# Kernel optimization log

Measured on AMD Instinct MI355X. Metric: run time of the kernel, lower is better.

The kernel has to match this reference:

```python
import jax, jax.numpy as jnp
import numpy as np

B, S, E, H = 2, 512, 1024, 16
D = E // H  # 64


def setup_inputs() -> dict:
    key = jax.random.key(0)
    ks = jax.random.split(key, 8)
    q = jax.random.normal(ks[0], (B, S, E), dtype=jnp.float32)
    k = jax.random.normal(ks[1], (B, S, E), dtype=jnp.float32)
    v = jax.random.normal(ks[2], (B, S, E), dtype=jnp.float32)
    # per-position bilinear term, scaled down so scores stay in a sane range
    p = jax.random.normal(ks[3], (B, S, H, D, D), dtype=jnp.float32) * 0.05
    # causal additive mask [S, S]
    neg = jnp.float32(-1e9)
    mask = jnp.where(jnp.triu(jnp.ones((S, S), dtype=bool), k=1), neg, jnp.float32(0.0))
    scale = 1.0 / np.sqrt(E)
    Wq = jax.random.normal(ks[4], (E, E), dtype=jnp.float32) * scale
    Wk = jax.random.normal(ks[5], (E, E), dtype=jnp.float32) * scale
    Wv = jax.random.normal(ks[6], (E, E), dtype=jnp.float32) * scale
    Wo = jax.random.normal(ks[7], (E, E), dtype=jnp.float32) * scale
    return {"q": q, "k": k, "v": v, "p": p, "mask": mask,
            "Wq": Wq, "Wk": Wk, "Wv": Wv, "Wo": Wo}


def reference(q, k, v, p, mask, Wq, Wk, Wv, Wo):
    b, s, e = q.shape
    h, d = p.shape[2], p.shape[3]
    # projections (torch Linear: y = x @ W.T), split into heads -> [b,h,s,d]
    qh = (q @ Wq.T).reshape(b, s, h, d).transpose(0, 2, 1, 3)
    kh = (k @ Wk.T).reshape(b, -1, h, d).transpose(0, 2, 1, 3)
    vh = (v @ Wv.T).reshape(b, -1, h, d).transpose(0, 2, 1, 3)
    # scores = einsum('bhse,bshef,bhtf->bhst') done in two steps
    qp = jnp.einsum('bhse,bshef->bhsf', qh, p)          # [b,h,s,d]
    scores = jnp.einsum('bhsf,bhtf->bhst', qp, kh)      # [b,h,s,t]
    scores = scores / jnp.sqrt(jnp.float32(d))
    scores = scores + mask[None, None, :, :]
    w = jax.nn.softmax(scores, axis=-1)
    att = jnp.einsum('bhst,bhtd->bshd', w, vh).reshape(b, s, e)
    return att @ Wo.T
```

## Files before the change

kernel.cpp:

```cpp
#include <hip/hip_runtime.h>
#include <hip/hip_bf16.h>

namespace {

constexpr int kB = 2, kS = 512, kE = 1024, kH = 16, kD = 64;
constexpr int kM = kB * kS;
constexpr int kBH = kB * kH;
constexpr int kSP = 524;

typedef short bf16x8 __attribute__((ext_vector_type(8)));
typedef float f32x4 __attribute__((ext_vector_type(4)));

__device__ __forceinline__ unsigned short f2bf(float f) {
  __hip_bfloat16 h = __float2bfloat16(f);
  unsigned short u;
  __builtin_memcpy(&u, &h, 2);
  return u;
}
__device__ __forceinline__ float bf2f(unsigned short u) {
  unsigned int x = (unsigned int)u << 16;
  float f;
  __builtin_memcpy(&f, &x, 4);
  return f;
}

__global__ void cvt7_kernel(const float* __restrict__ s0, const float* __restrict__ s1,
                            const float* __restrict__ s2, const float* __restrict__ s3,
                            const float* __restrict__ s4, const float* __restrict__ s5,
                            const float* __restrict__ s6,
                            unsigned short* __restrict__ dstBase) {
  const float* srcs[7] = {s0, s1, s2, s3, s4, s5, s6};
  const float* src = srcs[blockIdx.y];
  unsigned short* dst = dstBase + (size_t)blockIdx.y * (kM * kE);
  int i = (blockIdx.x * blockDim.x + threadIdx.x) * 4;
  float4 v = *reinterpret_cast<const float4*>(src + i);
  ushort4 o;
  o.x = f2bf(v.x); o.y = f2bf(v.y); o.z = f2bf(v.z); o.w = f2bf(v.w);
  *reinterpret_cast<ushort4*>(dst + i) = o;
}

__device__ __forceinline__ void mfma_tile_32x32(
    const unsigned short* __restrict__ A, int lda,
    const unsigned short* __restrict__ Bm, int ldb,
    int row0, int col0, int K, f32x4 acc[2][2]) {
  const int lane = threadIdx.x & 63;
  const int r = lane & 15;
  const int ko = (lane >> 4) * 8;
  const unsigned short* a0 = A + (size_t)(row0 + r) * lda + ko;
  const unsigned short* a1 = a0 + 16 * (size_t)lda;
  const unsigned short* b0 = Bm + (size_t)(col0 + r) * ldb + ko;
  const unsigned short* b1 = b0 + 16 * (size_t)ldb;
  for (int kk = 0; kk < K; kk += 32) {
    bf16x8 af0 = *reinterpret_cast<const bf16x8*>(a0 + kk);
    bf16x8 af1 = *reinterpret_cast<const bf16x8*>(a1 + kk);
    bf16x8 bg0 = *reinterpret_cast<const bf16x8*>(b0 + kk);
    bf16x8 bg1 = *reinterpret_cast<const bf16x8*>(b1 + kk);
    acc[0][0] = __builtin_amdgcn_mfma_f32_16x16x32_bf16(af0, bg0, acc[0][0], 0, 0, 0);
    acc[0][1] = __builtin_amdgcn_mfma_f32_16x16x32_bf16(af0, bg1, acc[0][1], 0, 0, 0);
    acc[1][0] = __builtin_amdgcn_mfma_f32_16x16x32_bf16(af1, bg0, acc[1][0], 0, 0, 0);
    acc[1][1] = __builtin_amdgcn_mfma_f32_16x16x32_bf16(af1, bg1, acc[1][1], 0, 0, 0);
  }
}

__global__ void proj_kernel(const unsigned short* __restrict__ qb,
                            const unsigned short* __restrict__ kb,
                            const unsigned short* __restrict__ vb,
                            const unsigned short* __restrict__ Wq,
                            const unsigned short* __restrict__ Wk,
                            const unsigned short* __restrict__ Wv,
                            unsigned short* __restrict__ qh,
                            unsigned short* __restrict__ kh,
                            unsigned short* __restrict__ vhT) {
  const int which = blockIdx.z;
  const unsigned short* A = which == 0 ? qb : (which == 1 ? kb : vb);
  const unsigned short* W = which == 0 ? Wq : (which == 1 ? Wk : Wv);
  const int row0 = blockIdx.y * 32, col0 = blockIdx.x * 32;
  f32x4 acc[2][2] = {};
  mfma_tile_32x32(A, kE, W, kE, row0, col0, kE, acc);
  const int lane = threadIdx.x & 63;
#pragma unroll
  for (int ri = 0; ri < 2; ++ri)
#pragma unroll
    for (int ci = 0; ci < 2; ++ci)
#pragma unroll
      for (int r = 0; r < 4; ++r) {
        int i = row0 + 16 * ri + 4 * (lane >> 4) + r;
        int j = col0 + 16 * ci + (lane & 15);
        int b = i >> 9, s = i & 511, h = j >> 6, d = j & 63;
        unsigned short val = f2bf(acc[ri][ci][r]);
        if (which == 2)
          vhT[(((size_t)(b * kH + h) * kD) + d) * kS + s] = val;
        else if (which == 1)
          kh[(((size_t)(b * kH + h) * kS) + s) * kD + d] = val;
        else
          qh[(((size_t)(b * kH + h) * kS) + s) * kD + d] = val;
      }
}

__global__ void qp_kernel(const float* __restrict__ p,
                          const unsigned short* __restrict__ qh,
                          unsigned short* __restrict__ qp) {
  __shared__ float qsh[kH][kD];
  const int bs = blockIdx.x;
  const int b = bs >> 9, s = bs & 511;
  const int t = threadIdx.x;
  {
    int h = t >> 4, d4 = (t & 15) * 4;
    const unsigned short* qr =
        qh + (((size_t)(b * kH + h) * kS) + s) * kD + d4;
    ushort4 u = *reinterpret_cast<const ushort4*>(qr);
    qsh[h][d4 + 0] = bf2f(u.x);
    qsh[h][d4 + 1] = bf2f(u.y);
    qsh[h][d4 + 2] = bf2f(u.z);
    qsh[h][d4 + 3] = bf2f(u.w);
  }
  __syncthreads();
  const int h = t >> 4, fi = t & 15;
  const float4* p4 =
      reinterpret_cast<const float4*>(p + ((size_t)(bs * kH + h) << 12));
  float4 acc = {0.f, 0.f, 0.f, 0.f};
#pragma unroll 4
  for (int e = 0; e < kD; ++e) {
    float4 pv = p4[e * 16 + fi];
    float qv = qsh[h][e];
    acc.x += qv * pv.x;
    acc.y += qv * pv.y;
    acc.z += qv * pv.z;
    acc.w += qv * pv.w;
  }
  ushort4 o;
  o.x = f2bf(acc.x); o.y = f2bf(acc.y); o.z = f2bf(acc.z); o.w = f2bf(acc.w);
  *reinterpret_cast<ushort4*>(
      qp + (((size_t)(b * kH + h) * kS) + s) * kD + fi * 4) = o;
}

__global__ __launch_bounds__(256) void attn_kernel(
    const unsigned short* __restrict__ qp,
    const unsigned short* __restrict__ kh,
    const unsigned short* __restrict__ vhT,
    unsigned short* __restrict__ att) {
  __shared__ float S[32 * kSP];
  const int bh = blockIdx.y;
  const int b = bh >> 4, h = bh & 15;
  const int bx = blockIdx.x;
  const int row0 = bx * 32;
  const int ncol = row0 + 32;
  const int w = threadIdx.x >> 6;
  const int lane = threadIdx.x & 63;
  const int g = lane >> 4, c = lane & 15;

  const unsigned short* Abase = qp + (size_t)bh * kS * kD;
  const unsigned short* Kbase = kh + (size_t)bh * kS * kD;

  bf16x8 qa[2][2];
#pragma unroll
  for (int ri = 0; ri < 2; ++ri)
#pragma unroll
    for (int kk = 0; kk < 2; ++kk)
      qa[ri][kk] = *reinterpret_cast<const bf16x8*>(
          Abase + (size_t)(row0 + 16 * ri + c) * kD + kk * 32 + g * 8);

  for (int ct = w; ct <= bx; ct += 4) {
    const int col0 = ct * 32;
    const unsigned short* kr0 = Kbase + (size_t)(col0 + c) * kD + g * 8;
    bf16x8 kb00 = *reinterpret_cast<const bf16x8*>(kr0);
    bf16x8 kb01 = *reinterpret_cast<const bf16x8*>(kr0 + 32);
    bf16x8 kb10 = *reinterpret_cast<const bf16x8*>(kr0 + 16 * kD);
    bf16x8 kb11 = *reinterpret_cast<const bf16x8*>(kr0 + 16 * kD + 32);
    f32x4 sacc[2][2] = {};
    sacc[0][0] = __builtin_amdgcn_mfma_f32_16x16x32_bf16(qa[0][0], kb00, sacc[0][0], 0, 0, 0);
    sacc[0][0] = __builtin_amdgcn_mfma_f32_16x16x32_bf16(qa[0][1], kb01, sacc[0][0], 0, 0, 0);
    sacc[0][1] = __builtin_amdgcn_mfma_f32_16x16x32_bf16(qa[0][0], kb10, sacc[0][1], 0, 0, 0);
    sacc[0][1] = __builtin_amdgcn_mfma_f32_16x16x32_bf16(qa[0][1], kb11, sacc[0][1], 0, 0, 0);
    sacc[1][0] = __builtin_amdgcn_mfma_f32_16x16x32_bf16(qa[1][0], kb00, sacc[1][0], 0, 0, 0);
    sacc[1][0] = __builtin_amdgcn_mfma_f32_16x16x32_bf16(qa[1][1], kb01, sacc[1][0], 0, 0, 0);
    sacc[1][1] = __builtin_amdgcn_mfma_f32_16x16x32_bf16(qa[1][0], kb10, sacc[1][1], 0, 0, 0);
    sacc[1][1] = __builtin_amdgcn_mfma_f32_16x16x32_bf16(qa[1][1], kb11, sacc[1][1], 0, 0, 0);
#pragma unroll
    for (int ri = 0; ri < 2; ++ri)
#pragma unroll
      for (int ci = 0; ci < 2; ++ci)
#pragma unroll
        for (int r = 0; r < 4; ++r) {
          int il = 16 * ri + 4 * g + r;
          int jg = col0 + 16 * ci + c;
          float val = sacc[ri][ci][r] * 0.125f;
          if (jg > row0 + il) val = -1e9f;
          S[il * kSP + jg] = val;
        }
  }
  __syncthreads();

#pragma unroll
  for (int rr = 0; rr < 8; ++rr) {
    const int i = w * 8 + rr;
    float v[8];
    float m = -1e30f;
#pragma unroll
    for (int ii = 0; ii < 8; ++ii) {
      int j = lane + 64 * ii;
      v[ii] = (j < ncol) ? S[i * kSP + j] : -1e30f;
      m = fmaxf(m, v[ii]);
    }
#pragma unroll
    for (int off = 32; off; off >>= 1) m = fmaxf(m, __shfl_xor(m, off));
    float e[8], sum = 0.f;
#pragma unroll
    for (int ii = 0; ii < 8; ++ii) {
      e[ii] = __expf(v[ii] - m);
      sum += e[ii];
    }
#pragma unroll
    for (int off = 32; off; off >>= 1) sum += __shfl_xor(sum, off);
    const float inv = 1.0f / sum;
#pragma unroll
    for (int ii = 0; ii < 8; ++ii) S[i * kSP + lane + 64 * ii] = e[ii] * inv;
  }
  __syncthreads();

  const int d0 = w * 16;
  const unsigned short* Vbase = vhT + (size_t)(bh * kD + d0 + c) * kS;
  f32x4 oacc[2] = {};
  const int nk = bx + 1;
  for (int ks = 0; ks < nk; ++ks) {
    const int kb = ks * 32;
    bf16x8 vfrag = *reinterpret_cast<const bf16x8*>(Vbase + kb + g * 8);
#pragma unroll
    for (int ri = 0; ri < 2; ++ri) {
      const float* sp = &S[(16 * ri + c) * kSP + kb + g * 8];
      float4 x0 = *reinterpret_cast<const float4*>(sp);
      float4 x1 = *reinterpret_cast<const float4*>(sp + 4);
      bf16x8 pa;
      pa[0] = (short)f2bf(x0.x); pa[1] = (short)f2bf(x0.y);
      pa[2] = (short)f2bf(x0.z); pa[3] = (short)f2bf(x0.w);
      pa[4] = (short)f2bf(x1.x); pa[5] = (short)f2bf(x1.y);
      pa[6] = (short)f2bf(x1.z); pa[7] = (short)f2bf(x1.w);
      oacc[ri] = __builtin_amdgcn_mfma_f32_16x16x32_bf16(pa, vfrag, oacc[ri], 0, 0, 0);
    }
  }
#pragma unroll
  for (int ri = 0; ri < 2; ++ri)
#pragma unroll
    for (int r = 0; r < 4; ++r) {
      int s = row0 + 16 * ri + 4 * g + r;
      int d = d0 + c;
      att[((size_t)(b * kS + s) * kE) + h * kD + d] = f2bf(oacc[ri][r]);
    }
}

__global__ void out_kernel(const unsigned short* __restrict__ att,
                           const unsigned short* __restrict__ Wo,
                           float* __restrict__ out) {
  const int row0 = blockIdx.y * 32, col0 = blockIdx.x * 32;
  f32x4 acc[2][2] = {};
  mfma_tile_32x32(att, kE, Wo, kE, row0, col0, kE, acc);
  const int lane = threadIdx.x & 63;
#pragma unroll
  for (int ri = 0; ri < 2; ++ri)
#pragma unroll
    for (int ci = 0; ci < 2; ++ci)
#pragma unroll
      for (int r = 0; r < 4; ++r) {
        int i = row0 + 16 * ri + 4 * (lane >> 4) + r;
        int j = col0 + 16 * ci + (lane & 15);
        out[(size_t)i * kE + j] = acc[ri][ci][r];
      }
}

}

extern "C" void kernel_launch(void* const* d_in, const int* in_sizes, int n_in,
                              void* d_out, int out_size, void* d_ws,
                              size_t ws_size, hipStream_t stream) {
  const float* q = (const float*)d_in[0];
  const float* k = (const float*)d_in[1];
  const float* v = (const float*)d_in[2];
  const float* p = (const float*)d_in[3];
  const float* Wq = (const float*)d_in[5];
  const float* Wk = (const float*)d_in[6];
  const float* Wv = (const float*)d_in[7];
  const float* Wo = (const float*)d_in[8];
  float* out = (float*)d_out;

  char* ws = (char*)d_ws;
  size_t off = 0;
  auto alloc = [&](size_t bytes) {
    void* ptr = ws + off;
    off += (bytes + 255) & ~(size_t)255;
    return ptr;
  };
  const size_t nME = (size_t)kM * kE;
  unsigned short* qb = (unsigned short*)alloc(nME * 2);
  unsigned short* kb = (unsigned short*)alloc(nME * 2);
  unsigned short* vb = (unsigned short*)alloc(nME * 2);
  unsigned short* Wqb = (unsigned short*)alloc(nME * 2);
  unsigned short* Wkb = (unsigned short*)alloc(nME * 2);
  unsigned short* Wvb = (unsigned short*)alloc(nME * 2);
  unsigned short* Wob = (unsigned short*)alloc(nME * 2);
  unsigned short* qhB = (unsigned short*)alloc(nME * 2);
  unsigned short* khB = (unsigned short*)alloc(nME * 2);
  unsigned short* vhTB = (unsigned short*)alloc(nME * 2);
  unsigned short* qpB = (unsigned short*)alloc(nME * 2);
  unsigned short* attB = (unsigned short*)alloc(nME * 2);

  cvt7_kernel<<<dim3(kM * kE / (256 * 4), 7), 256, 0, stream>>>(
      q, k, v, Wq, Wk, Wv, Wo, qb);

  proj_kernel<<<dim3(kE / 32, kM / 32, 3), 64, 0, stream>>>(
      qb, kb, vb, Wqb, Wkb, Wvb, qhB, khB, vhTB);

  qp_kernel<<<kB * kS, 256, 0, stream>>>(p, qhB, qpB);

  attn_kernel<<<dim3(kS / 32, kBH), 256, 0, stream>>>(qpB, khB, vhTB, attB);

  out_kernel<<<dim3(kE / 32, kM / 32), 64, 0, stream>>>(attB, Wob, out);
}
```

Baseline: 146.0 us.

## Overlap K/V projections with the bilinear qp step in one kernel

Splits the Q projection into its own kernel. The K and V projection tiles are interleaved with the per-position bilinear qp work inside a single launch, so the p-bandwidth-bound qp blocks run concurrently with the MFMA-bound projection blocks. GEMM kernels also move from 64-thread blocks to 256-thread blocks, each covering a 64x64 tile with four waves. This trades some branch divergence and uneven block costs within the merged launch for fewer launches and better overlap of memory and compute.

```diff
diff --git a/kernel.cpp b/kernel.cpp
--- a/kernel.cpp
+++ b/kernel.cpp
@@ -62,21 +62,14 @@
   }
 }
 
-__global__ void proj_kernel(const unsigned short* __restrict__ qb,
-                            const unsigned short* __restrict__ kb,
-                            const unsigned short* __restrict__ vb,
-                            const unsigned short* __restrict__ Wq,
-                            const unsigned short* __restrict__ Wk,
-                            const unsigned short* __restrict__ Wv,
-                            unsigned short* __restrict__ qh,
-                            unsigned short* __restrict__ kh,
-                            unsigned short* __restrict__ vhT) {
-  const int which = blockIdx.z;
-  const unsigned short* A = which == 0 ? qb : (which == 1 ? kb : vb);
-  const unsigned short* W = which == 0 ? Wq : (which == 1 ? Wk : Wv);
-  const int row0 = blockIdx.y * 32, col0 = blockIdx.x * 32;
+__global__ __launch_bounds__(256) void proj_q_kernel(
+    const unsigned short* __restrict__ qb, const unsigned short* __restrict__ Wq,
+    unsigned short* __restrict__ qh) {
+  const int w = threadIdx.x >> 6;
+  const int row0 = blockIdx.y * 64 + (w >> 1) * 32;
+  const int col0 = blockIdx.x * 64 + (w & 1) * 32;
   f32x4 acc[2][2] = {};
-  mfma_tile_32x32(A, kE, W, kE, row0, col0, kE, acc);
+  mfma_tile_32x32(qb, kE, Wq, kE, row0, col0, kE, acc);
   const int lane = threadIdx.x & 63;
 #pragma unroll
   for (int ri = 0; ri < 2; ++ri)
@@ -87,51 +80,79 @@
         int i = row0 + 16 * ri + 4 * (lane >> 4) + r;
         int j = col0 + 16 * ci + (lane & 15);
         int b = i >> 9, s = i & 511, h = j >> 6, d = j & 63;
-        unsigned short val = f2bf(acc[ri][ci][r]);
-        if (which == 2)
-          vhT[(((size_t)(b * kH + h) * kD) + d) * kS + s] = val;
-        else if (which == 1)
-          kh[(((size_t)(b * kH + h) * kS) + s) * kD + d] = val;
-        else
-          qh[(((size_t)(b * kH + h) * kS) + s) * kD + d] = val;
+        qh[(((size_t)(b * kH + h) * kS) + s) * kD + d] = f2bf(acc[ri][ci][r]);
       }
 }
 
-__global__ void qp_kernel(const float* __restrict__ p,
-                          const unsigned short* __restrict__ qh,
-                          unsigned short* __restrict__ qp) {
+__global__ __launch_bounds__(256) void mega_kernel(
+    const float* __restrict__ p, const unsigned short* __restrict__ qh,
+    unsigned short* __restrict__ qp,
+    const unsigned short* __restrict__ kb, const unsigned short* __restrict__ vb,
+    const unsigned short* __restrict__ Wk, const unsigned short* __restrict__ Wv,
+    unsigned short* __restrict__ kh, unsigned short* __restrict__ vhT) {
   __shared__ float qsh[kH][kD];
-  const int bs = blockIdx.x;
-  const int b = bs >> 9, s = bs & 511;
-  const int t = threadIdx.x;
-  {
-    int h = t >> 4, d4 = (t & 15) * 4;
-    const unsigned short* qr =
-        qh + (((size_t)(b * kH + h) * kS) + s) * kD + d4;
-    ushort4 u = *reinterpret_cast<const ushort4*>(qr);
-    qsh[h][d4 + 0] = bf2f(u.x);
-    qsh[h][d4 + 1] = bf2f(u.y);
-    qsh[h][d4 + 2] = bf2f(u.z);
-    qsh[h][d4 + 3] = bf2f(u.w);
-  }
-  __syncthreads();
-  const int h = t >> 4, fi = t & 15;
-  const float4* p4 =
-      reinterpret_cast<const float4*>(p + ((size_t)(bs * kH + h) << 12));
-  float4 acc = {0.f, 0.f, 0.f, 0.f};
+  const int flat = blockIdx.x;
+  const int mod = flat % 3;
+  if (mod == 2) {
+    const int pidx = flat / 3;
+    const int which = pidx >> 8;
+    const int tile = pidx & 255;
+    const int w = threadIdx.x >> 6;
+    const int row0 = (tile >> 4) * 64 + (w >> 1) * 32;
+    const int col0 = (tile & 15) * 64 + (w & 1) * 32;
+    const unsigned short* A = which ? vb : kb;
+    const unsigned short* W = which ? Wv : Wk;
+    f32x4 acc[2][2] = {};
+    mfma_tile_32x32(A, kE, W, kE, row0, col0, kE, acc);
+    const int lane = threadIdx.x & 63;
+#pragma unroll
+    for (int ri = 0; ri < 2; ++ri)
+#pragma unroll
+      for (int ci = 0; ci < 2; ++ci)
+#pragma unroll
+        for (int r = 0; r < 4; ++r) {
+          int i = row0 + 16 * ri + 4 * (lane >> 4) + r;
+          int j = col0 + 16 * ci + (lane & 15);
+          int b = i >> 9, s = i & 511, h = j >> 6, d = j & 63;
+          unsigned short val = f2bf(acc[ri][ci][r]);
+          if (which)
+            vhT[(((size_t)(b * kH + h) * kD) + d) * kS + s] = val;
+          else
+            kh[(((size_t)(b * kH + h) * kS) + s) * kD + d] = val;
+        }
+  } else {
+    const int bs = (flat / 3) * 2 + mod;
+    const int b = bs >> 9, s = bs & 511;
+    const int t = threadIdx.x;
+    {
+      int h = t >> 4, d4 = (t & 15) * 4;
+      const unsigned short* qr =
+          qh + (((size_t)(b * kH + h) * kS) + s) * kD + d4;
+      ushort4 u = *reinterpret_cast<const ushort4*>(qr);
+      qsh[h][d4 + 0] = bf2f(u.x);
+      qsh[h][d4 + 1] = bf2f(u.y);
+      qsh[h][d4 + 2] = bf2f(u.z);
+      qsh[h][d4 + 3] = bf2f(u.w);
+    }
+    __syncthreads();
+    const int h = t >> 4, fi = t & 15;
+    const float4* p4 =
+        reinterpret_cast<const float4*>(p + ((size_t)(bs * kH + h) << 12));
+    float4 acc = {0.f, 0.f, 0.f, 0.f};
 #pragma unroll 4
-  for (int e = 0; e < kD; ++e) {
-    float4 pv = p4[e * 16 + fi];
-    float qv = qsh[h][e];
-    acc.x += qv * pv.x;
-    acc.y += qv * pv.y;
-    acc.z += qv * pv.z;
-    acc.w += qv * pv.w;
-  }
-  ushort4 o;
-  o.x = f2bf(acc.x); o.y = f2bf(acc.y); o.z = f2bf(acc.z); o.w = f2bf(acc.w);
-  *reinterpret_cast<ushort4*>(
-      qp + (((size_t)(b * kH + h) * kS) + s) * kD + fi * 4) = o;
+    for (int e = 0; e < kD; ++e) {
+      float4 pv = p4[e * 16 + fi];
+      float qv = qsh[h][e];
+      acc.x += qv * pv.x;
+      acc.y += qv * pv.y;
+      acc.z += qv * pv.z;
+      acc.w += qv * pv.w;
+    }
+    ushort4 o;
+    o.x = f2bf(acc.x); o.y = f2bf(acc.y); o.z = f2bf(acc.z); o.w = f2bf(acc.w);
+    *reinterpret_cast<ushort4*>(
+        qp + (((size_t)(b * kH + h) * kS) + s) * kD + fi * 4) = o;
+  }
 }
 
 __global__ __launch_bounds__(256) void attn_kernel(
@@ -248,10 +269,12 @@
     }
 }
 
-__global__ void out_kernel(const unsigned short* __restrict__ att,
-                           const unsigned short* __restrict__ Wo,
-                           float* __restrict__ out) {
-  const int row0 = blockIdx.y * 32, col0 = blockIdx.x * 32;
+__global__ __launch_bounds__(256) void out_kernel(
+    const unsigned short* __restrict__ att, const unsigned short* __restrict__ Wo,
+    float* __restrict__ out) {
+  const int w = threadIdx.x >> 6;
+  const int row0 = blockIdx.y * 64 + (w >> 1) * 32;
+  const int col0 = blockIdx.x * 64 + (w & 1) * 32;
   f32x4 acc[2][2] = {};
   mfma_tile_32x32(att, kE, Wo, kE, row0, col0, kE, acc);
   const int lane = threadIdx.x & 63;
@@ -306,12 +329,12 @@
   cvt7_kernel<<<dim3(kM * kE / (256 * 4), 7), 256, 0, stream>>>(
       q, k, v, Wq, Wk, Wv, Wo, qb);
 
-  proj_kernel<<<dim3(kE / 32, kM / 32, 3), 64, 0, stream>>>(
-      qb, kb, vb, Wqb, Wkb, Wvb, qhB, khB, vhTB);
-
-  qp_kernel<<<kB * kS, 256, 0, stream>>>(p, qhB, qpB);
+  proj_q_kernel<<<dim3(kE / 64, kM / 64), 256, 0, stream>>>(qb, Wqb, qhB);
+
+  mega_kernel<<<1536, 256, 0, stream>>>(p, qhB, qpB, kb, vb, Wkb, Wvb, khB,
+                                        vhTB);
 
   attn_kernel<<<dim3(kS / 32, kBH), 256, 0, stream>>>(qpB, khB, vhTB, attB);
 
-  out_kernel<<<dim3(kE / 32, kM / 32), 64, 0, stream>>>(attB, Wob, out);
-}
+  out_kernel<<<dim3(kE / 64, kM / 64), 256, 0, stream>>>(attB, Wob, out);
+}
```

Result: no change. 144.6 us (-1.0%).
